# Kernel tuning notes

Hardware: AMD Instinct MI355X
Metric: run time of the kernel (lower is better)

The kernel has to match this reference:

```python
import jax, jax.numpy as jnp
import numpy as np

# Sizes (match init_kwargs / input_specs)
N, D, H, E = 4096, 512, 2048, 8   # tokens, dim, hidden_dim, num_experts
DK = 2                             # dynamic_k = top_k(3) - fixed_k(1)
NC = E - 1                         # dynamic candidate count (experts 1..7)
BETA_FIXED = 1.0 / 3.0             # fixed_k / top_k
BETA_DYN = 2.0 / 3.0               # dynamic_k / top_k


def setup_inputs() -> dict:
    key = jax.random.key(0)
    ks = jax.random.split(key, 5)
    def init(k, shape, fan_in):
        return jax.random.normal(k, shape, jnp.float32) * (1.0 / np.sqrt(fan_in))
    return {
        "x": jax.random.normal(ks[0], (N, D), jnp.float32),
        "router_W": init(ks[1], (D, NC), D),      # Linear(dim, num_non_fixed)
        "router_b": jnp.zeros((NC,), jnp.float32),
        "W1": init(ks[2], (E, D, H), D),           # per-expert first Linear
        "b1": jnp.zeros((E, H), jnp.float32),
        "W2": init(ks[3], (E, H, D), H),           # per-expert second Linear
        "b2": jnp.zeros((E, D), jnp.float32),
        "fixed_w": jnp.ones((1,), jnp.float32),    # fixed_branch_weights
    }


def reference(x, router_W, router_b, W1, b1, W2, b2, fixed_w):
    # All-expert MLP computed once (dense grouped-GEMM form of the
    # per-expert gather/MLP/scatter loop in the torch module).
    h = jax.nn.relu(jnp.einsum("nd,edh->neh", x, W1) + b1)   # [N,E,H]
    y = jnp.einsum("neh,ehd->ned", h, W2) + b2               # [N,E,D]

    # Fixed branch: expert 0 with fixed weight.
    fixed_out = fixed_w[0] * y[:, 0]                          # [N,D]

    # Dynamic branch: router over the 7 non-fixed experts.
    logits = x @ router_W + router_b                          # [N,NC]
    top_logits, top_idx = jax.lax.top_k(logits, DK)           # [N,DK]
    gates = jax.nn.softmax(top_logits, axis=-1)               # [N,DK]
    sel_expert = top_idx + 1                                  # lookup non_fixed [1..7]

    # combine weights per (token, expert): scatter gates via one-hot.
    combine = jnp.sum(jax.nn.one_hot(sel_expert, E, dtype=x.dtype)
                      * gates[..., None], axis=1)             # [N,E]
    dyn_out = jnp.einsum("ned,ne->nd", y, combine)            # [N,D]

    mixed = BETA_FIXED * fixed_out + BETA_DYN * dyn_out

    # Aux losses (same math as torch).
    importance = jax.nn.softmax(logits, axis=-1).mean(axis=0)  # [NC]
    uniform = 1.0 / NC
    load_balance_loss = jnp.mean((importance - uniform) ** 2)
    router_entropy = -jnp.sum(importance * jnp.log(jnp.clip(importance, 1e-8)))

    return mixed, load_balance_loss, router_entropy, sel_expert
```

## Files before the change

### kernel.cpp

```cpp
#include <hip/hip_runtime.h>
#include <math.h>

#define N_TOK 4096
#define DIM   512
#define HID   2048
#define NEXP  8
#define NC    7
#define OUT_MIXED (N_TOK*DIM)
#define TM    64

typedef __attribute__((ext_vector_type(8))) short bf16x8;
typedef __attribute__((ext_vector_type(4))) float f32x4;

#define XSP 520

#define OFF_XBF  262208ull
#define OFF_W1S  (OFF_XBF + 4194304ull)
#define OFF_W2S  (OFF_W1S + 16777216ull)
#define WS_REQ   (OFF_W2S + 16777216ull)

__device__ inline unsigned short f2bf(float f) {
  unsigned int u = __builtin_bit_cast(unsigned int, f);
  u = (u + 0x7fffu + ((u >> 16) & 1u)) >> 16;
  return (unsigned short)u;
}

template<int K, int Nm, int TILES_N>
__device__ void convert_w_body(const float* __restrict__ W,
                               unsigned int* __restrict__ Ws,
                               int blk, int tid,
                               unsigned short lds[32][264])
{
  const int e  = blk >> 7;
  const int rm = blk & 127;
  const int tk = rm / TILES_N;
  const int tn = rm - tk * TILES_N;

  const float* src = W + ((size_t)e * K + tk * 32) * Nm + tn * 256;
#pragma unroll
  for (int it = 0; it < 32; ++it) {
    const int i = it * 256 + tid;
    const int row = i >> 8, col = i & 255;
    lds[row][col] = f2bf(src[(size_t)row * Nm + col]);
  }
  __syncthreads();

  const int ntiles = Nm >> 4, kblks = K >> 3;
#pragma unroll
  for (int it = 0; it < 16; ++it) {
    const int uid   = it * 256 + tid;
    const int nt_l  = uid >> 8;
    const int r     = uid & 255;
    const int kb_l  = r >> 6;
    const int u     = r & 63;
    const int n_lo  = u >> 2;
    const int k_hf  = u & 3;
    const int d_l   = kb_l * 8 + k_hf * 2;
    const int h_l   = nt_l * 16 + n_lo;
    const unsigned int s0 = lds[d_l][h_l], s1 = lds[d_l + 1][h_l];
    const int nt_g = tn * 16 + nt_l;
    const int kb_g = tk * 4 + kb_l;
    const size_t frag = ((size_t)e * ntiles + nt_g) * kblks + kb_g;
    Ws[frag * 64 + n_lo * 4 + k_hf] = s0 | (s1 << 16);
  }
}

__global__ __launch_bounds__(256) void prep_kernel(
    const float* __restrict__ x, const float* __restrict__ rW,
    const float* __restrict__ rb, float* __restrict__ out,
    int* __restrict__ cpad, float* __restrict__ ipad,
    int* __restrict__ tok_list, float* __restrict__ wt_list,
    unsigned short* __restrict__ xbf,
    const float* __restrict__ W1, unsigned int* __restrict__ W1s,
    const float* __restrict__ W2, unsigned int* __restrict__ W2s)
{
  __shared__ unsigned short clds[32][264];
  __shared__ float imp_loc[8];
  __shared__ int   cnt_loc[8];
  __shared__ int   ltok[8][32];
  __shared__ float lwt[8][32];
  __shared__ int   base_s[8];

  const int b   = blockIdx.x;
  const int tid = threadIdx.x;

  if (b < 1024) {
    const int g = b * 256 + tid;
    const float* src = x + (size_t)g * 8;
    unsigned short tmp[8];
#pragma unroll
    for (int j = 0; j < 8; ++j) tmp[j] = f2bf(src[j]);
    *(uint4*)(xbf + (size_t)g * 8) = *(const uint4*)tmp;
    return;
  }
  if (b < 2048) { convert_w_body< 512, 2048, 8>(W1, W1s, b - 1024, tid, clds); return; }
  if (b < 3072) { convert_w_body<2048,  512, 2>(W2, W2s, b - 2048, tid, clds); return; }

  const int rb_ = b - 3072;

  {
    const float4 z = {0.f, 0.f, 0.f, 0.f};
    float4* o4 = (float4*)out + (size_t)rb_ * 2048;
    for (int i = tid; i < 2048; i += 256) o4[i] = z;
  }

  if (tid < 8) { imp_loc[tid] = 0.f; cnt_loc[tid] = 0; }
  __syncthreads();
  const int wave = tid >> 6, lane = tid & 63;

  for (int it = 0; it < 4; ++it) {
    const int t = rb_ * 16 + wave * 4 + it;
    float xv[8];
#pragma unroll
    for (int j = 0; j < 8; ++j) xv[j] = x[(size_t)t*DIM + lane + 64*j];
    float lg[NC];
#pragma unroll
    for (int e = 0; e < NC; ++e) {
      float s = 0.f;
#pragma unroll
      for (int j = 0; j < 8; ++j) s += xv[j] * rW[(lane + 64*j)*NC + e];
      lg[e] = s;
    }
#pragma unroll
    for (int e = 0; e < NC; ++e) {
      float s = lg[e];
#pragma unroll
      for (int off = 32; off > 0; off >>= 1) s += __shfl_xor(s, off, 64);
      lg[e] = s + rb[e];
    }
    int i1 = 0; float l1 = lg[0];
#pragma unroll
    for (int e = 1; e < NC; ++e) { if (lg[e] > l1) { l1 = lg[e]; i1 = e; } }
    int i2 = -1; float l2 = -3.4e38f;
#pragma unroll
    for (int e = 0; e < NC; ++e) { if (e != i1 && lg[e] > l2) { l2 = lg[e]; i2 = e; } }

    const float ed = expf(l2 - l1);
    const float g1 = 1.f/(1.f+ed), g2 = ed/(1.f+ed);

    float p[NC]; float ssum = 0.f;
#pragma unroll
    for (int e = 0; e < NC; ++e) { p[e] = expf(lg[e] - l1); ssum += p[e]; }
    const float inv = 1.f/ssum;

    if (lane == 0) {
#pragma unroll
      for (int e = 0; e < NC; ++e) atomicAdd(&imp_loc[e], p[e]*inv);
      out[OUT_MIXED + 2 + 2*t]     = (float)(i1 + 1);
      out[OUT_MIXED + 2 + 2*t + 1] = (float)(i2 + 1);
      const int e1 = i1 + 1, e2 = i2 + 1;
      int p1 = atomicAdd(&cnt_loc[e1], 1);
      ltok[e1][p1] = t;  lwt[e1][p1] = (2.f/3.f)*g1;
      int p2 = atomicAdd(&cnt_loc[e2], 1);
      ltok[e2][p2] = t;  lwt[e2][p2] = (2.f/3.f)*g2;
    }
  }
  __syncthreads();

  if (tid >= 1 && tid < 8)
    base_s[tid] = atomicAdd(&cpad[tid * 32], cnt_loc[tid]);
  if (tid < NC)
    atomicAdd(&ipad[(tid + 1) * 32], imp_loc[tid]);
  __syncthreads();

  {
    const int e = tid >> 5, i = tid & 31;
    if (e >= 1 && i < cnt_loc[e]) {
      const int dst = e * N_TOK + base_s[e] + i;
      tok_list[dst] = ltok[e][i];
      wt_list [dst] = lwt[e][i];
    }
  }

  __threadfence();
  __syncthreads();
  if (tid == 0) {
    if (atomicAdd(&cpad[0], 1) == 255) {
      float lb = 0.f, ent = 0.f;
      for (int ee = 0; ee < NC; ++ee) {
        float p = atomicAdd(&ipad[(ee + 1) * 32], 0.f) * (1.f/(float)N_TOK);
        float d = p - (1.f/(float)NC);
        lb += d*d;
        ent -= p * logf(fmaxf(p, 1e-8f));
      }
      out[OUT_MIXED]     = lb * (1.f/(float)NC);
      out[OUT_MIXED + 1] = ent;
    }
  }
}

__global__ __launch_bounds__(512, 2) void moe_mlp_mfma(
    const unsigned short* __restrict__ xbf,
    const unsigned short* __restrict__ W1s,
    const unsigned short* __restrict__ W2s,
    const float* __restrict__ b1, const float* __restrict__ b2,
    const float* __restrict__ fixed_w,
    const int* __restrict__ cpad, const int* __restrict__ tok_list,
    const float* __restrict__ wt_list, float* __restrict__ out)
{
  const int b = blockIdx.x;
  int e, tile, half;
  if (b < 256) {
    const int rho = b & 7, u = b >> 3;
    const int quota = (rho < 6) ? 11 : 31;
    if (u >= quota) return;
    const int prefix = (rho < 6) ? rho * 11 : (rho == 6 ? 66 : 97);
    const int unit = prefix + u;
    e = 0; half = unit >> 6; tile = unit & 63;
  } else {
    const int v = b - 256;
    const int rho = v & 7, u = v >> 3;
    const int cls = ((u >> 6) << 3) + rho;
    if (cls >= 14) return;
    e = (cls >> 1) + 1; half = cls & 1; tile = u & 63;
  }
  const int cnt   = (e == 0) ? N_TOK : cpad[e * 32];
  const int start = tile * TM;
  if (start >= cnt) return;

  __shared__ __align__(16) unsigned short xs[TM * XSP];
  __shared__ __align__(16) unsigned short hs[TM * XSP];
  __shared__ int   tok_s[TM];
  __shared__ float wt_s[TM];

  const int tid = threadIdx.x;
  if (tid < TM) {
    int idx = start + tid; int t = 0; float wv = 0.f;
    if (idx < cnt) {
      if (e == 0) { t = idx; wv = (1.f/3.f) * fixed_w[0]; }
      else        { t = tok_list[e*N_TOK + idx]; wv = wt_list[e*N_TOK + idx]; }
    }
    tok_s[tid] = t; wt_s[tid] = wv;
  }
  __syncthreads();

  for (int i = tid; i < TM * 64; i += 512) {
    const int m = i >> 6, cb = i & 63;
    *(uint4*)(xs + m * XSP + cb * 8) =
        *(const uint4*)(xbf + (size_t)tok_s[m] * DIM + cb * 8);
  }

  const int lane = tid & 63;
  const int wn   = tid >> 6;
  const int l15  = lane & 15;
  const int q    = lane >> 4;

  const unsigned short* W1e = W1s + (size_t)e * 128 * 64 * 128;
  const unsigned short* W2e = W2s + (size_t)e * 32 * 256 * 128;

  f32x4 yacc[4][4];
#pragma unroll
  for (int mi = 0; mi < 4; ++mi)
#pragma unroll
    for (int t = 0; t < 4; ++t) yacc[mi][t] = (f32x4){0.f, 0.f, 0.f, 0.f};

  __syncthreads();

  for (int ch = 0; ch < 2; ++ch) {
    const int ntb = half * 64 + ch * 32 + wn * 4;
    f32x4 hacc[4][4];
#pragma unroll
    for (int mi = 0; mi < 4; ++mi)
#pragma unroll
      for (int t = 0; t < 4; ++t) hacc[mi][t] = (f32x4){0.f, 0.f, 0.f, 0.f};
#pragma unroll 2
    for (int s = 0; s < 16; ++s) {
      bf16x8 a[4];
#pragma unroll
      for (int mi = 0; mi < 4; ++mi)
        a[mi] = *(const bf16x8*)(xs + (mi*16 + l15) * XSP + s * 32 + q * 8);
#pragma unroll
      for (int t = 0; t < 4; ++t) {
        const bf16x8 bb = *(const bf16x8*)(
            W1e + (((size_t)(ntb + t) * 64) + s * 4 + q) * 128 + l15 * 8);
#pragma unroll
        for (int mi = 0; mi < 4; ++mi)
          hacc[mi][t] = __builtin_amdgcn_mfma_f32_16x16x32_bf16(a[mi], bb, hacc[mi][t], 0, 0, 0);
      }
    }
#pragma unroll
    for (int t = 0; t < 4; ++t) {
      const float bv = b1[e * HID + (ntb + t) * 16 + l15];
      const int col = (wn * 4 + t) * 16 + l15;
#pragma unroll
      for (int mi = 0; mi < 4; ++mi)
#pragma unroll
        for (int reg = 0; reg < 4; ++reg)
          hs[(mi*16 + q*4 + reg) * XSP + col] =
              f2bf(fmaxf(hacc[mi][t][reg] + bv, 0.f));
    }
    __syncthreads();

    const int kb_base = half * 128 + ch * 64;
#pragma unroll 2
    for (int s = 0; s < 16; ++s) {
      bf16x8 a[4];
#pragma unroll
      for (int mi = 0; mi < 4; ++mi)
        a[mi] = *(const bf16x8*)(hs + (mi*16 + l15) * XSP + s * 32 + q * 8);
      const int kblk = kb_base + s * 4 + q;
#pragma unroll
      for (int t = 0; t < 4; ++t) {
        const bf16x8 bb = *(const bf16x8*)(
            W2e + (((size_t)(wn * 4 + t) * 256) + kblk) * 128 + l15 * 8);
#pragma unroll
        for (int mi = 0; mi < 4; ++mi)
          yacc[mi][t] = __builtin_amdgcn_mfma_f32_16x16x32_bf16(a[mi], bb, yacc[mi][t], 0, 0, 0);
      }
    }
    __syncthreads();
  }

#pragma unroll
  for (int t = 0; t < 4; ++t) {
    const int d = (wn * 4 + t) * 16 + l15;
    const float b2v = half ? 0.f : b2[e * DIM + d];
#pragma unroll
    for (int mi = 0; mi < 4; ++mi)
#pragma unroll
      for (int reg = 0; reg < 4; ++reg) {
        const int m = mi*16 + q*4 + reg;
        atomicAdd(&out[(size_t)tok_s[m] * DIM + d], wt_s[m] * (yacc[mi][t][reg] + b2v));
      }
  }
}

__global__ __launch_bounds__(256) void router_kernel(
    const float* __restrict__ x, const float* __restrict__ rW,
    const float* __restrict__ rb, float* __restrict__ out,
    int* __restrict__ cpad, float* __restrict__ ipad,
    int* __restrict__ tok_list, float* __restrict__ wt_list)
{
  __shared__ float imp_loc[8];
  __shared__ int   cnt_loc[8];
  __shared__ int   ltok[8][32];
  __shared__ float lwt[8][32];
  __shared__ int   base_s[8];

  const int tid = threadIdx.x;
  if (tid < 8) { imp_loc[tid] = 0.f; cnt_loc[tid] = 0; }
  __syncthreads();
  const int wave = tid >> 6, lane = tid & 63;

  for (int it = 0; it < 4; ++it) {
    const int t = blockIdx.x * 16 + wave * 4 + it;
    float xv[8];
#pragma unroll
    for (int j = 0; j < 8; ++j) xv[j] = x[(size_t)t*DIM + lane + 64*j];
    float lg[NC];
#pragma unroll
    for (int e = 0; e < NC; ++e) {
      float s = 0.f;
#pragma unroll
      for (int j = 0; j < 8; ++j) s += xv[j] * rW[(lane + 64*j)*NC + e];
      lg[e] = s;
    }
#pragma unroll
    for (int e = 0; e < NC; ++e) {
      float s = lg[e];
#pragma unroll
      for (int off = 32; off > 0; off >>= 1) s += __shfl_xor(s, off, 64);
      lg[e] = s + rb[e];
    }
    int i1 = 0; float l1 = lg[0];
#pragma unroll
    for (int e = 1; e < NC; ++e) { if (lg[e] > l1) { l1 = lg[e]; i1 = e; } }
    int i2 = -1; float l2 = -3.4e38f;
#pragma unroll
    for (int e = 0; e < NC; ++e) { if (e != i1 && lg[e] > l2) { l2 = lg[e]; i2 = e; } }

    const float ed = expf(l2 - l1);
    const float g1 = 1.f/(1.f+ed), g2 = ed/(1.f+ed);

    float p[NC]; float ssum = 0.f;
#pragma unroll
    for (int e = 0; e < NC; ++e) { p[e] = expf(lg[e] - l1); ssum += p[e]; }
    const float inv = 1.f/ssum;

    if (lane == 0) {
#pragma unroll
      for (int e = 0; e < NC; ++e) atomicAdd(&imp_loc[e], p[e]*inv);
      out[OUT_MIXED + 2 + 2*t]     = (float)(i1 + 1);
      out[OUT_MIXED + 2 + 2*t + 1] = (float)(i2 + 1);
      const int e1 = i1 + 1, e2 = i2 + 1;
      int p1 = atomicAdd(&cnt_loc[e1], 1);
      ltok[e1][p1] = t;  lwt[e1][p1] = (2.f/3.f)*g1;
      int p2 = atomicAdd(&cnt_loc[e2], 1);
      ltok[e2][p2] = t;  lwt[e2][p2] = (2.f/3.f)*g2;
    }
  }
  __syncthreads();

  if (tid >= 1 && tid < 8)
    base_s[tid] = atomicAdd(&cpad[tid * 32], cnt_loc[tid]);
  if (tid < NC)
    atomicAdd(&ipad[(tid + 1) * 32], imp_loc[tid]);
  __syncthreads();

  {
    const int e = tid >> 5, i = tid & 31;
    if (e >= 1 && i < cnt_loc[e]) {
      const int dst = e * N_TOK + base_s[e] + i;
      tok_list[dst] = ltok[e][i];
      wt_list [dst] = lwt[e][i];
    }
  }
}

__global__ void finalize_kernel(const float* __restrict__ ipad,
                                float* __restrict__ out)
{
  if (threadIdx.x == 0 && blockIdx.x == 0) {
    float lb = 0.f, ent = 0.f;
    for (int e = 0; e < NC; ++e) {
      float p = ipad[(e + 1) * 32] * (1.f/(float)N_TOK);
      float d = p - (1.f/(float)NC);
      lb += d*d;
      ent -= p * logf(fmaxf(p, 1e-8f));
    }
    out[OUT_MIXED]     = lb * (1.f/(float)NC);
    out[OUT_MIXED + 1] = ent;
  }
}

__global__ __launch_bounds__(256) void moe_mlp_kernel(
    const float* __restrict__ x,
    const float* __restrict__ W1, const float* __restrict__ b1,
    const float* __restrict__ W2, const float* __restrict__ b2,
    const float* __restrict__ fixed_w,
    const int* __restrict__ cpad, const int* __restrict__ tok_list,
    const float* __restrict__ wt_list, float* __restrict__ out)
{
  const int e    = blockIdx.x >> 8;
  const int tile = blockIdx.x & 255;
  const int cnt  = (e == 0) ? N_TOK : cpad[e * 32];
  const int start = tile * 16;
  if (start >= cnt) return;

  __shared__ float xs[DIM][17];
  __shared__ float hs2[256][17];
  __shared__ int   tok_s[16];
  __shared__ float wt_s[16];

  const int tid = threadIdx.x;
  if (tid < 16) {
    int idx = start + tid; int t = 0; float w = 0.f;
    if (idx < cnt) {
      if (e == 0) { t = idx; w = (1.f/3.f) * fixed_w[0]; }
      else        { t = tok_list[e*N_TOK + idx]; w = wt_list[e*N_TOK + idx]; }
    }
    tok_s[tid] = t; wt_s[tid] = w;
  }
  __syncthreads();

  for (int i = tid; i < 16*DIM; i += 256) {
    const int m = i >> 9, d = i & (DIM-1);
    xs[d][m] = x[(size_t)tok_s[m]*DIM + d];
  }

  const int r  = tid & 63;
  const int m0 = (tid >> 6) * 4;
  const float* W1e = W1 + (size_t)e * DIM * HID;
  const float* W2e = W2 + (size_t)e * HID * DIM;
  const float* b1e = b1 + e * HID;

  float yacc[4][8];
#pragma unroll
  for (int j = 0; j < 4; ++j)
#pragma unroll
    for (int i = 0; i < 8; ++i) yacc[j][i] = 0.f;

  __syncthreads();

  for (int c = 0; c < 8; ++c) {
    const int k0 = c * 256;
    float bv[4];
#pragma unroll
    for (int i = 0; i < 4; ++i) bv[i] = b1e[k0 + r + 64*i];
    float hacc[4][4];
#pragma unroll
    for (int j = 0; j < 4; ++j)
#pragma unroll
      for (int i = 0; i < 4; ++i) hacc[j][i] = bv[i];
#pragma unroll 2
    for (int d = 0; d < DIM; ++d) {
      float wv[4];
#pragma unroll
      for (int i = 0; i < 4; ++i) wv[i] = W1e[(size_t)d*HID + k0 + r + 64*i];
      float xv[4];
#pragma unroll
      for (int j = 0; j < 4; ++j) xv[j] = xs[d][m0+j];
#pragma unroll
      for (int j = 0; j < 4; ++j)
#pragma unroll
        for (int i = 0; i < 4; ++i) hacc[j][i] += xv[j]*wv[i];
    }
#pragma unroll
    for (int i = 0; i < 4; ++i)
#pragma unroll
      for (int j = 0; j < 4; ++j) hs2[r + 64*i][m0+j] = fmaxf(hacc[j][i], 0.f);
    __syncthreads();

#pragma unroll 2
    for (int k = 0; k < 256; ++k) {
      float wv2[8];
#pragma unroll
      for (int i = 0; i < 8; ++i) wv2[i] = W2e[(size_t)(k0+k)*DIM + r + 64*i];
      float hv[4];
#pragma unroll
      for (int j = 0; j < 4; ++j) hv[j] = hs2[k][m0+j];
#pragma unroll
      for (int j = 0; j < 4; ++j)
#pragma unroll
        for (int i = 0; i < 8; ++i) yacc[j][i] += hv[j]*wv2[i];
    }
    __syncthreads();
  }

#pragma unroll
  for (int i = 0; i < 8; ++i) {
    const int d = r + 64*i;
    const float b2v = b2[e*DIM + d];
#pragma unroll
    for (int j = 0; j < 4; ++j) {
      const int m = m0 + j;
      atomicAdd(&out[(size_t)tok_s[m]*DIM + d], wt_s[m]*(yacc[j][i] + b2v));
    }
  }
}

extern "C" void kernel_launch(void* const* d_in, const int* in_sizes, int n_in,
                              void* d_out, int out_size, void* d_ws, size_t ws_size,
                              hipStream_t stream)
{
  const float* x  = (const float*)d_in[0];
  const float* rW = (const float*)d_in[1];
  const float* rb = (const float*)d_in[2];
  const float* W1 = (const float*)d_in[3];
  const float* b1 = (const float*)d_in[4];
  const float* W2 = (const float*)d_in[5];
  const float* b2 = (const float*)d_in[6];
  const float* fw = (const float*)d_in[7];
  float* out = (float*)d_out;

  int*   tok_list = (int*)((char*)d_ws + 64);
  float* wt_list  = (float*)((char*)d_ws + 64 + (size_t)NEXP*N_TOK*4);
  int*   cpad     = tok_list;
  float* ipad     = (float*)((char*)tok_list + 1024);

  hipMemsetAsync(cpad, 0, 2048, stream);

  if (ws_size >= WS_REQ) {
    unsigned short* xbf = (unsigned short*)((char*)d_ws + OFF_XBF);
    unsigned int*   W1s = (unsigned int*)((char*)d_ws + OFF_W1S);
    unsigned int*   W2s = (unsigned int*)((char*)d_ws + OFF_W2S);
    prep_kernel<<<3328, 256, 0, stream>>>(x, rW, rb, out, cpad, ipad,
                                          tok_list, wt_list, xbf,
                                          W1, W1s, W2, W2s);
    moe_mlp_mfma<<<1280, 512, 0, stream>>>(xbf, (const unsigned short*)W1s,
                                           (const unsigned short*)W2s, b1, b2, fw,
                                           cpad, tok_list, wt_list, out);
  } else {
    hipMemsetAsync(d_out, 0, (size_t)OUT_MIXED*4, stream);
    router_kernel<<<256, 256, 0, stream>>>(x, rW, rb, out, cpad, ipad,
                                           tok_list, wt_list);
    finalize_kernel<<<1, 64, 0, stream>>>(ipad, out);
    moe_mlp_kernel<<<NEXP*256, 256, 0, stream>>>(x, W1, b1, W2, b2, fw,
                                                 cpad, tok_list, wt_list, out);
  }
}
```

Before: 310.8 us.

## Use 1024-thread blocks covering full hidden dim and prefetch weight fragments

The MLP kernel moves to 1024-thread blocks with 16 waves split 2x8 over tokens and output columns. Each block now covers the full hidden dimension in four chunks rather than splitting it in half across two blocks. This removes the duplicated x-tile loads and halves the atomic adds to the output. Weight fragments are register double-buffered one k-step ahead, and the per-wave token tile shrinks from 64 to 32 rows. The trade-offs are fewer blocks (768), heavier work per block, and a launch-bounds request of four 1024-thread blocks per CU that shared memory probably cannot meet.

After: 333.6 us. 1.07x slower.

```diff
diff --git a/kernel.cpp b/kernel.cpp
--- a/kernel.cpp
+++ b/kernel.cpp
@@ -189,7 +189,7 @@
   }
 }
 
-__global__ __launch_bounds__(512, 2) void moe_mlp_mfma(
+__global__ __launch_bounds__(1024, 4) void moe_mlp_mfma(
     const unsigned short* __restrict__ xbf,
     const unsigned short* __restrict__ W1s,
     const unsigned short* __restrict__ W2s,
@@ -199,20 +199,18 @@
     const float* __restrict__ wt_list, float* __restrict__ out)
 {
   const int b = blockIdx.x;
-  int e, tile, half;
+  int e, tile;
   if (b < 256) {
     const int rho = b & 7, u = b >> 3;
-    const int quota = (rho < 6) ? 11 : 31;
+    const int quota = (rho < 7) ? 5 : 29;
     if (u >= quota) return;
-    const int prefix = (rho < 6) ? rho * 11 : (rho == 6 ? 66 : 97);
-    const int unit = prefix + u;
-    e = 0; half = unit >> 6; tile = unit & 63;
+    const int prefix = (rho < 7) ? rho * 5 : 35;
+    e = 0; tile = prefix + u;
   } else {
     const int v = b - 256;
-    const int rho = v & 7, u = v >> 3;
-    const int cls = ((u >> 6) << 3) + rho;
-    if (cls >= 14) return;
-    e = (cls >> 1) + 1; half = cls & 1; tile = u & 63;
+    const int rho = v & 7;
+    if (rho >= 7) return;
+    e = rho + 1; tile = v >> 3;
   }
   const int cnt   = (e == 0) ? N_TOK : cpad[e * 32];
   const int start = tile * TM;
@@ -234,92 +232,109 @@
   }
   __syncthreads();
 
-  for (int i = tid; i < TM * 64; i += 512) {
+  for (int i = tid; i < TM * 64; i += 1024) {
     const int m = i >> 6, cb = i & 63;
     *(uint4*)(xs + m * XSP + cb * 8) =
         *(const uint4*)(xbf + (size_t)tok_s[m] * DIM + cb * 8);
   }
 
   const int lane = tid & 63;
-  const int wn   = tid >> 6;
+  const int w    = tid >> 6;
+  const int wn   = w & 7;
+  const int wm   = w >> 3;
   const int l15  = lane & 15;
   const int q    = lane >> 4;
 
   const unsigned short* W1e = W1s + (size_t)e * 128 * 64 * 128;
   const unsigned short* W2e = W2s + (size_t)e * 32 * 256 * 128;
 
-  f32x4 yacc[4][4];
-#pragma unroll
-  for (int mi = 0; mi < 4; ++mi)
+  f32x4 yacc[2][4];
+#pragma unroll
+  for (int mi = 0; mi < 2; ++mi)
 #pragma unroll
     for (int t = 0; t < 4; ++t) yacc[mi][t] = (f32x4){0.f, 0.f, 0.f, 0.f};
 
-  __syncthreads();
-
-  for (int ch = 0; ch < 2; ++ch) {
-    const int ntb = half * 64 + ch * 32 + wn * 4;
-    f32x4 hacc[4][4];
-#pragma unroll
-    for (int mi = 0; mi < 4; ++mi)
+  const int r0 = wm * 32 + l15;
+  const int r1 = wm * 32 + 16 + l15;
+
+  __syncthreads();
+
+#define W1ADDR(t, s) (const bf16x8*)(W1e + (((size_t)(ntb + (t)) * 64) + (s) * 4 + q) * 128 + l15 * 8)
+#define W2ADDR(t, s) (const bf16x8*)(W2e + (((size_t)(wn * 4 + (t)) * 256) + ch * 64 + (s) * 4 + q) * 128 + l15 * 8)
+
+  for (int ch = 0; ch < 4; ++ch) {
+    const int ntb = ch * 32 + wn * 4;
+    f32x4 hacc[2][4];
+#pragma unroll
+    for (int mi = 0; mi < 2; ++mi)
 #pragma unroll
       for (int t = 0; t < 4; ++t) hacc[mi][t] = (f32x4){0.f, 0.f, 0.f, 0.f};
-#pragma unroll 2
+
+    bf16x8 bc0 = *W1ADDR(0, 0), bc1 = *W1ADDR(1, 0),
+           bc2 = *W1ADDR(2, 0), bc3 = *W1ADDR(3, 0);
+#pragma unroll
     for (int s = 0; s < 16; ++s) {
-      bf16x8 a[4];
-#pragma unroll
-      for (int mi = 0; mi < 4; ++mi)
-        a[mi] = *(const bf16x8*)(xs + (mi*16 + l15) * XSP + s * 32 + q * 8);
-#pragma unroll
-      for (int t = 0; t < 4; ++t) {
-        const bf16x8 bb = *(const bf16x8*)(
-            W1e + (((size_t)(ntb + t) * 64) + s * 4 + q) * 128 + l15 * 8);
-#pragma unroll
-        for (int mi = 0; mi < 4; ++mi)
-          hacc[mi][t] = __builtin_amdgcn_mfma_f32_16x16x32_bf16(a[mi], bb, hacc[mi][t], 0, 0, 0);
-      }
+      bf16x8 bn0, bn1, bn2, bn3;
+      if (s < 15) { bn0 = *W1ADDR(0, s+1); bn1 = *W1ADDR(1, s+1);
+                    bn2 = *W1ADDR(2, s+1); bn3 = *W1ADDR(3, s+1); }
+      const bf16x8 a0 = *(const bf16x8*)(xs + r0 * XSP + s * 32 + q * 8);
+      const bf16x8 a1 = *(const bf16x8*)(xs + r1 * XSP + s * 32 + q * 8);
+      hacc[0][0] = __builtin_amdgcn_mfma_f32_16x16x32_bf16(a0, bc0, hacc[0][0], 0, 0, 0);
+      hacc[1][0] = __builtin_amdgcn_mfma_f32_16x16x32_bf16(a1, bc0, hacc[1][0], 0, 0, 0);
+      hacc[0][1] = __builtin_amdgcn_mfma_f32_16x16x32_bf16(a0, bc1, hacc[0][1], 0, 0, 0);
+      hacc[1][1] = __builtin_amdgcn_mfma_f32_16x16x32_bf16(a1, bc1, hacc[1][1], 0, 0, 0);
+      hacc[0][2] = __builtin_amdgcn_mfma_f32_16x16x32_bf16(a0, bc2, hacc[0][2], 0, 0, 0);
+      hacc[1][2] = __builtin_amdgcn_mfma_f32_16x16x32_bf16(a1, bc2, hacc[1][2], 0, 0, 0);
+      hacc[0][3] = __builtin_amdgcn_mfma_f32_16x16x32_bf16(a0, bc3, hacc[0][3], 0, 0, 0);
+      hacc[1][3] = __builtin_amdgcn_mfma_f32_16x16x32_bf16(a1, bc3, hacc[1][3], 0, 0, 0);
+      bc0 = bn0; bc1 = bn1; bc2 = bn2; bc3 = bn3;
     }
 #pragma unroll
     for (int t = 0; t < 4; ++t) {
       const float bv = b1[e * HID + (ntb + t) * 16 + l15];
       const int col = (wn * 4 + t) * 16 + l15;
 #pragma unroll
-      for (int mi = 0; mi < 4; ++mi)
+      for (int mi = 0; mi < 2; ++mi)
 #pragma unroll
         for (int reg = 0; reg < 4; ++reg)
-          hs[(mi*16 + q*4 + reg) * XSP + col] =
+          hs[(wm*32 + mi*16 + q*4 + reg) * XSP + col] =
               f2bf(fmaxf(hacc[mi][t][reg] + bv, 0.f));
     }
     __syncthreads();
 
-    const int kb_base = half * 128 + ch * 64;
-#pragma unroll 2
+    bf16x8 cc0 = *W2ADDR(0, 0), cc1 = *W2ADDR(1, 0),
+           cc2 = *W2ADDR(2, 0), cc3 = *W2ADDR(3, 0);
+#pragma unroll
     for (int s = 0; s < 16; ++s) {
-      bf16x8 a[4];
-#pragma unroll
-      for (int mi = 0; mi < 4; ++mi)
-        a[mi] = *(const bf16x8*)(hs + (mi*16 + l15) * XSP + s * 32 + q * 8);
-      const int kblk = kb_base + s * 4 + q;
-#pragma unroll
-      for (int t = 0; t < 4; ++t) {
-        const bf16x8 bb = *(const bf16x8*)(
-            W2e + (((size_t)(wn * 4 + t) * 256) + kblk) * 128 + l15 * 8);
-#pragma unroll
-        for (int mi = 0; mi < 4; ++mi)
-          yacc[mi][t] = __builtin_amdgcn_mfma_f32_16x16x32_bf16(a[mi], bb, yacc[mi][t], 0, 0, 0);
-      }
+      bf16x8 cn0, cn1, cn2, cn3;
+      if (s < 15) { cn0 = *W2ADDR(0, s+1); cn1 = *W2ADDR(1, s+1);
+                    cn2 = *W2ADDR(2, s+1); cn3 = *W2ADDR(3, s+1); }
+      const bf16x8 a0 = *(const bf16x8*)(hs + r0 * XSP + s * 32 + q * 8);
+      const bf16x8 a1 = *(const bf16x8*)(hs + r1 * XSP + s * 32 + q * 8);
+      yacc[0][0] = __builtin_amdgcn_mfma_f32_16x16x32_bf16(a0, cc0, yacc[0][0], 0, 0, 0);
+      yacc[1][0] = __builtin_amdgcn_mfma_f32_16x16x32_bf16(a1, cc0, yacc[1][0], 0, 0, 0);
+      yacc[0][1] = __builtin_amdgcn_mfma_f32_16x16x32_bf16(a0, cc1, yacc[0][1], 0, 0, 0);
+      yacc[1][1] = __builtin_amdgcn_mfma_f32_16x16x32_bf16(a1, cc1, yacc[1][1], 0, 0, 0);
+      yacc[0][2] = __builtin_amdgcn_mfma_f32_16x16x32_bf16(a0, cc2, yacc[0][2], 0, 0, 0);
+      yacc[1][2] = __builtin_amdgcn_mfma_f32_16x16x32_bf16(a1, cc2, yacc[1][2], 0, 0, 0);
+      yacc[0][3] = __builtin_amdgcn_mfma_f32_16x16x32_bf16(a0, cc3, yacc[0][3], 0, 0, 0);
+      yacc[1][3] = __builtin_amdgcn_mfma_f32_16x16x32_bf16(a1, cc3, yacc[1][3], 0, 0, 0);
+      cc0 = cn0; cc1 = cn1; cc2 = cn2; cc3 = cn3;
     }
     __syncthreads();
   }
+#undef W1ADDR
+#undef W2ADDR
 
 #pragma unroll
   for (int t = 0; t < 4; ++t) {
     const int d = (wn * 4 + t) * 16 + l15;
-    const float b2v = half ? 0.f : b2[e * DIM + d];
-#pragma unroll
-    for (int mi = 0; mi < 4; ++mi)
+    const float b2v = b2[e * DIM + d];
+#pragma unroll
+    for (int mi = 0; mi < 2; ++mi)
 #pragma unroll
       for (int reg = 0; reg < 4; ++reg) {
-        const int m = mi*16 + q*4 + reg;
+        const int m = wm*32 + mi*16 + q*4 + reg;
         atomicAdd(&out[(size_t)tok_s[m] * DIM + d], wt_s[m] * (yacc[mi][t][reg] + b2v));
       }
   }
@@ -557,7 +572,7 @@
     prep_kernel<<<3328, 256, 0, stream>>>(x, rW, rb, out, cpad, ipad,
                                           tok_list, wt_list, xbf,
                                           W1, W1s, W2, W2s);
-    moe_mlp_mfma<<<1280, 512, 0, stream>>>(xbf, (const unsigned short*)W1s,
+    moe_mlp_mfma<<<768, 1024, 0, stream>>>(xbf, (const unsigned short*)W1s,
                                            (const unsigned short*)W2s, b1, b2, fw,
                                            cpad, tok_list, wt_list, out);
   } else {
```
